# Kernel tuning notes

Measured on AMD Instinct MI355X. Metric: run time of the kernel, lower is better.

The kernel has to match this reference:

```python
import jax, jax.numpy as jnp
import numpy as np

B, C, D, J = 8, 2048, 128, 128

def setup_inputs() -> dict:
    key = jax.random.key(0)
    ks = jax.random.split(key, 24)
    s = 0.02
    inp = {
        "operation_features": jax.random.normal(ks[0], (B, C, D), jnp.float32),
        "relations": jax.random.randint(ks[1], (B, C - 2, 2), 0, C, jnp.int64),
        "begins_idx": jax.random.randint(ks[2], (B, J), 0, C, jnp.int64),
        "ends_idx": jax.random.randint(ks[3], (B, J), 0, C, jnp.int64),
        "same_type_mask": (jax.random.uniform(ks[4], (B, C, C)) > 0.5).astype(jnp.float32),
        # BeginEndEncoder
        "W_begin": jax.random.normal(ks[5], (D, D), jnp.float32) * s,
        "b_begin": jnp.zeros((D,), jnp.float32),
        "W_end": jax.random.normal(ks[6], (D, D), jnp.float32) * s,
        "b_end": jnp.zeros((D,), jnp.float32),
        # OperationTimeRelationEncoder.mix: Linear(3D -> D)
        "W_mix3": jax.random.normal(ks[7], (3 * D, D), jnp.float32) * s,
        "b_mix3": jnp.zeros((D,), jnp.float32),
        # SelfAttention (hidden_dim = D)
        "W_qkv": jax.random.normal(ks[8], (D, 3 * D), jnp.float32) * s,
        "b_qkv": jnp.zeros((3 * D,), jnp.float32),
        "w_score": jax.random.normal(ks[9], (2 * D,), jnp.float32) * s,
        "b_score": jnp.zeros((), jnp.float32),
        "W_out": jax.random.normal(ks[10], (D, D), jnp.float32) * s,
        "b_out": jnp.zeros((D,), jnp.float32),
        # block mix: Linear(2D -> D)
        "W_mix2": jax.random.normal(ks[11], (2 * D, D), jnp.float32) * s,
        "b_mix2": jnp.zeros((D,), jnp.float32),
    }
    return inp

def _gather_ops(ops, idx):
    # ops: [B,C,D], idx: [B,M] -> [B,M,D]  (torch.gather along dim 1 with expanded index)
    Bb, _, Dd = ops.shape
    M = idx.shape[1]
    return jnp.take_along_axis(ops, jnp.broadcast_to(idx[:, :, None], (Bb, M, Dd)), axis=1)

def reference(operation_features, relations, begins_idx, ends_idx, same_type_mask,
              W_begin, b_begin, W_end, b_end, W_mix3, b_mix3,
              W_qkv, b_qkv, w_score, b_score, W_out, b_out, W_mix2, b_mix2):
    ops = operation_features
    Dd = ops.shape[-1]
    # --- OperationTimeRelationEncoder ---
    pred = _gather_ops(ops, relations[..., 0])      # [B,C-2,D]
    succ = _gather_ops(ops, relations[..., 1])      # [B,C-2,D]
    concated = jnp.concatenate([ops[:, :-2, :], pred, succ], axis=-1)  # [B,C-2,3D]
    mixed = concated @ W_mix3 + b_mix3              # [B,C-2,D]
    begin_f = _gather_ops(ops, begins_idx) @ W_begin + b_begin  # [B,J,D]
    end_f = _gather_ops(ops, ends_idx) @ W_end + b_end
    begin = jnp.mean(begin_f, axis=1)               # [B,D]
    end = jnp.mean(end_f, axis=1)
    seq = jnp.concatenate([mixed, begin[:, None, :], end[:, None, :]], axis=1)  # [B,C,D]
    # --- SelfAttention (GAT-style additive score, decomposed to avoid CxCx2h blowup) ---
    qkv = ops @ W_qkv + b_qkv                       # [B,C,3D]
    q, k, v = jnp.split(qkv, 3, axis=-1)
    sq = q @ w_score[:Dd]                           # [B,C]  q_i . w_q
    sk = k @ w_score[Dd:]                           # [B,C]  k_j . w_k
    scores = jax.nn.leaky_relu(sq[:, :, None] + sk[:, None, :] + b_score)  # [B,C,C]
    attn = jax.nn.softmax(scores * same_type_mask, axis=-1)                # multiplicative mask, as in torch
    weighted = jnp.einsum('bij,bjd->bid', attn, v)  # [B,C,D]
    same_type = weighted @ W_out + b_out            # [B,C,D]
    # --- final mix ---
    return jnp.concatenate([seq, same_type], axis=-1) @ W_mix2 + b_mix2  # [B,C,D]
```

## Files before the change

### kernel.cpp

```cpp
#include <hip/hip_runtime.h>
#include <cstddef>

typedef __bf16 bf16;
typedef __bf16 bf16x4 __attribute__((ext_vector_type(4)));
typedef __bf16 bf16x8 __attribute__((ext_vector_type(8)));
typedef float  f32x4  __attribute__((ext_vector_type(4)));

#define MFMA16(a, b, c) __builtin_amdgcn_mfma_f32_16x16x32_bf16((a), (b), (c), 0, 0, 0)

#define BB 8
#define CC 2048
#define DD 128
#define JJN 128

#define WS_PK    ((size_t)0)
#define WS_OATT  ((size_t)4194304)
#define WS_OPS16 ((size_t)8388608)
#define WS_SQF   ((size_t)12582912)
#define WS_SKF   ((size_t)12648448)
#define WS_G1T   ((size_t)12713984)
#define WS_G2T   ((size_t)12746752)
#define WS_G3T   ((size_t)12779520)
#define WS_WCT   ((size_t)12812288)
#define WS_GBT   ((size_t)12845056)
#define WS_GET   ((size_t)12877824)
#define WS_UQK   ((size_t)12910592)
#define WS_BBM   ((size_t)12911104)
#define WS_BBB   ((size_t)12911616)
#define WS_BBE   ((size_t)12912128)
#define WS_SC    ((size_t)12912640)
#define WS_WCN   ((size_t)12913152)
#define WS_GBN   ((size_t)12945920)
#define WS_GEN   ((size_t)12978688)
#define WS_MB    ((size_t)13011456)
#define WS_MEANV ((size_t)17205760)

__global__ __launch_bounds__(256) void k_prepcast(
    const float* __restrict__ ops, bf16* __restrict__ ops16,
    const float* __restrict__ mask, const int* __restrict__ begins,
    const int* __restrict__ ends,
    const float* __restrict__ Wmix3, const float* __restrict__ Wmix2,
    const float* __restrict__ Wout,  const float* __restrict__ Wbegin,
    const float* __restrict__ Wend,  const float* __restrict__ Wqkv,
    const float* __restrict__ bqkv,  const float* __restrict__ wscore,
    const float* __restrict__ bscore,const float* __restrict__ bmix3,
    const float* __restrict__ bout,  const float* __restrict__ bmix2,
    const float* __restrict__ bbegin,const float* __restrict__ bend,
    bf16* __restrict__ G1T, bf16* __restrict__ G2T, bf16* __restrict__ G3T,
    bf16* __restrict__ WCT, bf16* __restrict__ GBT, bf16* __restrict__ GET,
    bf16* __restrict__ WCN, bf16* __restrict__ GBN, bf16* __restrict__ GEN,
    bf16* __restrict__ uqk, float* __restrict__ BBM, float* __restrict__ BBB,
    float* __restrict__ BBE, float* __restrict__ sc,
    unsigned char* __restrict__ MBITS, float* __restrict__ MEANV)
{
    __shared__ bf16  LshT[128 * 132];
    __shared__ float Rsh[128 * 8];
    int wg = blockIdx.x;
    int t  = threadIdx.x;

    if (wg == 0) {
        for (int half = 0; half < 2; ++half) {
            #pragma unroll
            for (int pass = 0; pass < 16; ++pass) {
                int idx = pass * 256 + t;
                int d   = idx >> 5;
                int e0  = (idx & 31) * 4;
                f32x4 v = *(const f32x4*)(Wqkv + d*384 + half*128 + e0);
                #pragma unroll
                for (int jj = 0; jj < 4; ++jj)
                    LshT[(e0 + jj)*132 + d] = (bf16)v[jj];
            }
            if (t < 32) {
                f32x4 wv = *(const f32x4*)(wscore + half*128 + t*4);
                #pragma unroll
                for (int jj = 0; jj < 4; ++jj) Rsh[t*4 + jj] = wv[jj];
            }
            __syncthreads();
            if (t < 128) {
                float s = 0.f;
                for (int e = 0; e < 128; ++e)
                    s += (float)LshT[e*132 + t] * Rsh[e];
                uqk[half*128 + t] = (bf16)s;
            }
            __syncthreads();
        }
        float bm = 0.f, bb_ = 0.f, be_ = 0.f, bon = 0.f;
        for (int half = 0; half < 2; ++half) {
            #pragma unroll
            for (int pass = 0; pass < 16; ++pass) {
                int idx = pass * 256 + t;
                int f   = idx >> 5;
                int e0  = (idx & 31) * 4;
                f32x4 v = *(const f32x4*)(Wmix2 + (size_t)(half*128 + f)*128 + e0);
                #pragma unroll
                for (int jj = 0; jj < 4; ++jj)
                    LshT[f*132 + e0 + jj] = (bf16)v[jj];
            }
            if (t < 32) {
                if (half == 0) {
                    f32x4 v0 = *(const f32x4*)(bmix3  + t*4);
                    f32x4 v1 = *(const f32x4*)(bbegin + t*4);
                    f32x4 v2 = *(const f32x4*)(bend   + t*4);
                    #pragma unroll
                    for (int jj = 0; jj < 4; ++jj) {
                        Rsh[t*4 + jj]       = v0[jj];
                        Rsh[128 + t*4 + jj] = v1[jj];
                        Rsh[256 + t*4 + jj] = v2[jj];
                    }
                } else {
                    f32x4 v3 = *(const f32x4*)(bout + t*4);
                    #pragma unroll
                    for (int jj = 0; jj < 4; ++jj) Rsh[t*4 + jj] = v3[jj];
                }
            }
            __syncthreads();
            if (t < 128) {
                if (half == 0) {
                    for (int f = 0; f < 128; ++f) {
                        float wv = (float)LshT[f*132 + t];
                        bm  += Rsh[f]       * wv;
                        bb_ += Rsh[128 + f] * wv;
                        be_ += Rsh[256 + f] * wv;
                    }
                } else {
                    for (int f = 0; f < 128; ++f)
                        bon += Rsh[f] * (float)LshT[f*132 + t];
                }
            }
            __syncthreads();
        }
        if (t < 128) {
            float bm2 = bmix2[t];
            BBM[t] = bm  + bon + bm2;
            BBB[t] = bb_ + bon + bm2;
            BBE[t] = be_ + bon + bm2;
        }
        if (t >= 128) {
            int e2 = t - 128;
            Rsh[512 + e2] = bqkv[e2]       * wscore[e2];
            Rsh[640 + e2] = bqkv[128 + e2] * wscore[128 + e2];
        }
        __syncthreads();
        if (t == 0) {
            float cq = 0.f, ck = 0.f;
            for (int e2 = 0; e2 < 128; ++e2) {
                cq += Rsh[512 + e2];
                ck += Rsh[640 + e2];
            }
            sc[0] = cq + bscore[0];
            sc[1] = ck;
        }
        return;
    }
    if (wg <= 16) {
        int task = wg - 1;
        int b2 = task >> 1, which = task & 1;
        const int* idxp = which ? (ends + b2 * JJN) : (begins + b2 * JJN);
        int* ish = (int*)Rsh;
        if (t < JJN) ish[t] = idxp[t];
        __syncthreads();
        int d = t & 127, half = t >> 7;
        const float* opsb = ops + (size_t)b2 * CC * DD;
        float s = 0.f;
        #pragma unroll 8
        for (int j = 0; j < 64; ++j) {
            int r = ish[half * 64 + j];
            s += opsb[(size_t)r * DD + d];
        }
        float* fsh = Rsh + 256;
        fsh[half * 128 + d] = s;
        __syncthreads();
        if (t < 128)
            MEANV[task * 128 + t] = (fsh[t] + fsh[128 + t]) * (1.0f / (float)JJN);
        return;
    }
    if (wg <= 2064) {
        int p = wg - 17;
        size_t base = (size_t)p * 16384;
        const float* mp = mask + base;
        unsigned char* ob = MBITS + (base >> 3);
        #pragma unroll
        for (int k = 0; k < 8; ++k) {
            size_t fo = (size_t)k * 2048 + (size_t)t * 8;
            f32x4 a = __builtin_nontemporal_load((const f32x4*)(mp + fo));
            f32x4 c = __builtin_nontemporal_load((const f32x4*)(mp + fo + 4));
            unsigned byte = 0;
            #pragma unroll
            for (int e = 0; e < 4; ++e) {
                byte |= (a[e] != 0.f ? 1u : 0u) << e;
                byte |= (c[e] != 0.f ? 1u : 0u) << (4 + e);
            }
            ob[k * 256 + t] = (unsigned char)byte;
        }
        return;
    }
    if (wg <= 2160) {
        int id  = wg - 2065;
        int mat = id >> 4, sub = id & 15;
        const float* L; const float* R; bf16* O; bf16* O2;
        switch (mat) {
            case 0: L = Wmix3;           R = Wmix2;           O = G1T; O2 = nullptr; break;
            case 1: L = Wmix3 + 128*128; R = Wmix2;           O = G2T; O2 = nullptr; break;
            case 2: L = Wmix3 + 256*128; R = Wmix2;           O = G3T; O2 = nullptr; break;
            case 3: L = Wout;            R = Wmix2 + 128*128; O = WCT; O2 = WCN; break;
            case 4: L = Wbegin;          R = Wmix2;           O = GBT; O2 = GBN; break;
            default:L = Wend;            R = Wmix2;           O = GET; O2 = GEN; break;
        }
        int e0 = sub * 8;
        #pragma unroll
        for (int pass = 0; pass < 16; ++pass) {
            int idx = pass * 256 + t;
            int d   = idx >> 5;
            int f0  = (idx & 31) * 4;
            f32x4 v = *(const f32x4*)(L + d * 128 + f0);
            #pragma unroll
            for (int jj = 0; jj < 4; ++jj)
                LshT[(f0 + jj) * 132 + d] = (bf16)v[jj];
        }
        #pragma unroll
        for (int pass = 0; pass < 4; ++pass) {
            int idx = pass * 256 + t;
            int f   = idx >> 3;
            int ee  = idx & 7;
            Rsh[f * 8 + ee] = R[f * 128 + e0 + ee];
        }
        __syncthreads();
        int ee = t >> 5;
        int e  = e0 + ee;
        int d0 = (t & 31) * 4;
        float s[4] = {0.f, 0.f, 0.f, 0.f};
        for (int f = 0; f < 128; ++f) {
            bf16x4 lv = *(const bf16x4*)&LshT[f * 132 + d0];
            float rv = Rsh[f * 8 + ee];
            #pragma unroll
            for (int dd = 0; dd < 4; ++dd)
                s[dd] += (float)lv[dd] * rv;
        }
        #pragma unroll
        for (int dd = 0; dd < 4; ++dd) {
            O[e * 128 + d0 + dd] = (bf16)s[dd];
            if (O2) O2[(d0 + dd) * 128 + e] = (bf16)s[dd];
        }
        return;
    }
    size_t i = (size_t)(wg - 2161) * 256 + t;
    f32x4 a = *(const f32x4*)(ops + i * 8);
    f32x4 b = *(const f32x4*)(ops + i * 8 + 4);
    bf16x8 o;
    #pragma unroll
    for (int e = 0; e < 4; ++e) { o[e] = (bf16)a[e]; o[4 + e] = (bf16)b[e]; }
    *(bf16x8*)(ops16 + i * 8) = o;
}

__global__ __launch_bounds__(256) void k_v(
    const bf16* __restrict__ ops16, const float* __restrict__ Wqkv,
    const float* __restrict__ bqkv, const bf16* __restrict__ uqk,
    const float* __restrict__ sc,
    bf16* __restrict__ PK, float* __restrict__ sqf, float* __restrict__ skf)
{
    __shared__ bf16 A[144 * 136];
    int b  = blockIdx.x >> 4;
    int jt = (blockIdx.x & 15) * 128;
    int t  = threadIdx.x;
    #pragma unroll
    for (int pass = 0; pass < 16; ++pass) {
        int idx = pass * 256 + t;
        int d   = idx >> 5;
        int n0  = (idx & 31) * 4;
        f32x4 v = *(const f32x4*)(Wqkv + d*384 + 256 + n0);
        #pragma unroll
        for (int jj = 0; jj < 4; ++jj)
            A[(n0 + jj)*136 + d] = (bf16)v[jj];
    }
    {
        int row = t >> 7, col = t & 127;
        A[(128 + row)*136 + col] = uqk[row*128 + col];
    }
    for (int idx = t; idx < 14*136; idx += 256)
        A[130*136 + idx] = (bf16)0.f;
    __syncthreads();

    int lane = t & 63, w = t >> 6;
    int m = lane & 15, q = lane >> 4;
    f32x4 acc[9][2];
    #pragma unroll
    for (int rb = 0; rb < 9; ++rb)
        #pragma unroll
        for (int cb = 0; cb < 2; ++cb)
            acc[rb][cb] = {0.f, 0.f, 0.f, 0.f};

    const bf16* opsb = ops16 + (size_t)b * CC * DD;
    #pragma unroll
    for (int kc = 0; kc < 4; ++kc) {
        bf16x8 bfr[2];
        #pragma unroll
        for (int cb = 0; cb < 2; ++cb) {
            int j = jt + w*32 + cb*16 + m;
            bfr[cb] = *(const bf16x8*)(opsb + (size_t)j*DD + kc*32 + q*8);
        }
        #pragma unroll
        for (int rb = 0; rb < 9; ++rb) {
            bf16x8 afr = *(const bf16x8*)&A[(rb*16 + m)*136 + kc*32 + q*8];
            acc[rb][0] = MFMA16(afr, bfr[0], acc[rb][0]);
            acc[rb][1] = MFMA16(afr, bfr[1], acc[rb][1]);
        }
    }
    float cqb = sc[0], ckv = sc[1];
    #pragma unroll
    for (int cb = 0; cb < 2; ++cb) {
        int j = jt + w*32 + cb*16 + m;
        if (q == 0) {
            sqf[b*CC + j] = acc[8][cb][0] + cqb;
            skf[b*CC + j] = acc[8][cb][1] + ckv;
        }
    }
    __syncthreads();
    bf16* pack = A;
    #pragma unroll
    for (int cb = 0; cb < 2; ++cb) {
        int qq_base = cb*2 + (m>>3);
        int e       = m & 7;
        #pragma unroll
        for (int rb = 0; rb < 8; ++rb) {
            #pragma unroll
            for (int r = 0; r < 4; ++r) {
                float v = acc[rb][cb][r] + bqkv[256 + rb*16 + q*4 + r];
                pack[w*4096 + rb*512 + qq_base*128 + (q*4+r)*8 + e] = (bf16)v;
            }
        }
    }
    __syncthreads();
    bf16* pkb = PK + (size_t)b * DD * CC + (size_t)jt * 128;
    #pragma unroll
    for (int pass = 0; pass < 8; ++pass) {
        int lidx = pass * 256 + t;
        *(uint4*)(pkb + (size_t)lidx * 8) = *(const uint4*)&pack[lidx * 8];
    }
}

__device__ __forceinline__ void load_vb(const bf16* __restrict__ pkb, int jc,
                                        int q, int m, bf16x8 vb[8])
{
    #pragma unroll
    for (int nb = 0; nb < 8; ++nb)
        vb[nb] = *(const bf16x8*)(pkb + ((size_t)(((jc*8 + nb)*4 + q)*16 + m)) * 8);
}

__device__ __forceinline__ void substep(const float* __restrict__ skb,
    unsigned mbyte, int st, int sub, int q, float sq,
    const bf16x8 vb[8], float& lsum, f32x4 acc[8])
{
    int jo = st * 64 + sub * 32 + q * 8;
    f32x4 s0 = *(const f32x4*)(skb + jo);
    f32x4 s1 = *(const f32x4*)(skb + jo + 4);
    float sks[8] = {s0[0], s0[1], s0[2], s0[3], s1[0], s1[1], s1[2], s1[3]};
    bf16x8 a;
    #pragma unroll
    for (int e = 0; e < 8; ++e) {
        float tv = sq + sks[e];
        float lr = fmaxf(tv, 0.01f * tv);
        float pm = (float)((mbyte >> e) & 1u);
        float p  = __expf(lr * pm);
        lsum += p;
        a[e] = (bf16)p;
    }
    #pragma unroll
    for (int nb = 0; nb < 8; ++nb)
        acc[nb] = MFMA16(a, vb[nb], acc[nb]);
}

__global__ __launch_bounds__(256) void k_attepi(
    const unsigned char* __restrict__ MBITS, const bf16* __restrict__ PK,
    const float* __restrict__ sqf, const float* __restrict__ skf,
    const bf16* __restrict__ ops16, const int* __restrict__ relations,
    const bf16* __restrict__ G1T, const bf16* __restrict__ G2T,
    const bf16* __restrict__ G3T, const bf16* __restrict__ WCT,
    const bf16* __restrict__ GBN, const bf16* __restrict__ GEN,
    const bf16* __restrict__ WCN,
    const float* __restrict__ BBM, const float* __restrict__ BBB,
    const float* __restrict__ BBE, const float* __restrict__ MEANV,
    float* __restrict__ out)
{
    __shared__ __align__(16) char smem[52224];
    int t    = threadIdx.x;
    int lane = t & 63, w = t >> 6;
    int b    = blockIdx.x & 7;
    int i0   = (blockIdx.x >> 3) << 5;
    int m = lane & 15, q = lane >> 4;

    unsigned char* Lb  = (unsigned char*)smem;
    float*         skb = (float*)(smem + 8704 + w * 2048);

    {
        int row = t >> 3, seg = t & 7;
        const uint4* src = (const uint4*)(MBITS
            + ((size_t)(b * CC + i0 + row)) * 256 + seg * 32);
        uint4 v0 = src[0], v1 = src[1];
        *(uint4*)(Lb + row * 272 + seg * 32)      = v0;
        *(uint4*)(Lb + row * 272 + seg * 32 + 16) = v1;
    }
    {
        const float* src = skf + b * CC + w * 512;
        f32x4 v0 = *(const f32x4*)(src + lane * 4);
        f32x4 v1 = *(const f32x4*)(src + 256 + lane * 4);
        *(f32x4*)(skb + lane * 4)       = v0;
        *(f32x4*)(skb + 256 + lane * 4) = v1;
    }
    float sq0 = sqf[b * CC + i0 + m];
    float sq1 = sqf[b * CC + i0 + 16 + m];
    const bf16* pkb = PK + (size_t)b * DD * CC;
    int jc0 = w * 16;

    f32x4 acc0[8], acc1[8];
    #pragma unroll
    for (int nb = 0; nb < 8; ++nb) {
        acc0[nb] = {0.f, 0.f, 0.f, 0.f};
        acc1[nb] = {0.f, 0.f, 0.f, 0.f};
    }
    float lsum0 = 0.f, lsum1 = 0.f;
    __syncthreads();

    for (int st = 0; st < 8; ++st) {
        #pragma unroll
        for (int sub = 0; sub < 2; ++sub) {
            bf16x8 vb[8];
            load_vb(pkb, jc0 + st * 2 + sub, q, m, vb);
            int bo = w * 64 + st * 8 + sub * 4 + q;
            unsigned mb0 = Lb[m * 272 + bo];
            unsigned mb1 = Lb[(16 + m) * 272 + bo];
            substep(skb, mb0, st, sub, q, sq0, vb, lsum0, acc0);
            substep(skb, mb1, st, sub, q, sq1, vb, lsum1, acc1);
        }
    }

    __syncthreads();
    float* Osh  = (float*)(smem + 8704);
    float* Lsh  = (float*)(smem + 42496);
    bf16*  Obuf = (bf16*)(smem + 43520);
    #pragma unroll
    for (int tile = 0; tile < 2; ++tile) {
        float ls = tile ? lsum1 : lsum0;
        ls += __shfl_xor(ls, 16, 64);
        ls += __shfl_xor(ls, 32, 64);
        if (q == 0) Lsh[w * 16 + m] = ls;
        const f32x4* acc = tile ? acc1 : acc0;
        #pragma unroll
        for (int nb = 0; nb < 8; ++nb)
            #pragma unroll
            for (int r = 0; r < 4; ++r)
                Osh[(w * 16 + q * 4 + r) * 132 + nb * 16 + m] = acc[nb][r];
        __syncthreads();

        int r   = t >> 4;
        int c0e = (t & 15) * 8;
        float l = Lsh[r] + Lsh[16 + r] + Lsh[32 + r] + Lsh[48 + r];
        float inv = 1.0f / l;
        bf16x8 o;
        #pragma unroll
        for (int e = 0; e < 8; ++e) {
            float s = Osh[r * 132 + c0e + e] + Osh[(16 + r) * 132 + c0e + e]
                    + Osh[(32 + r) * 132 + c0e + e] + Osh[(48 + r) * 132 + c0e + e];
            o[e] = (bf16)(s * inv);
        }
        *(bf16x8*)&Obuf[(tile * 16 + r) * 136 + c0e] = o;
        __syncthreads();
    }

    bf16* Abuf = (bf16*)smem;
    bf16* Bbuf = (bf16*)(smem + 8704);

    f32x4 eacc[2][2];
    #pragma unroll
    for (int rb = 0; rb < 2; ++rb)
        #pragma unroll
        for (int cb = 0; cb < 2; ++cb)
            eacc[rb][cb] = {0.f, 0.f, 0.f, 0.f};

    const bf16* Bsrc[4] = {G1T, G2T, G3T, WCT};
    int arow = t >> 3, ao = (t & 7) * 16;
    int brow = t >> 1, bo2 = (t & 1) * 64;
    int c = i0 + arow;

    for (int term = 0; term < 4; ++term) {
        if (term < 3) {
            const bf16* src;
            if (term == 0) src = ops16 + ((size_t)(b * CC + c)) * DD;
            else {
                int ridx = relations[((size_t)b * (CC - 2) + min(c, CC - 3)) * 2 + (term - 1)];
                src = ops16 + ((size_t)(b * CC) + ridx) * DD;
            }
            *(uint4*)&Abuf[arow * 136 + ao]     = *(const uint4*)(src + ao);
            *(uint4*)&Abuf[arow * 136 + ao + 8] = *(const uint4*)(src + ao + 8);
        }
        const uint4* bs = (const uint4*)(Bsrc[term] + brow * 128 + bo2);
        uint4* bd = (uint4*)&Bbuf[brow * 136 + bo2];
        #pragma unroll
        for (int ii = 0; ii < 8; ++ii) bd[ii] = bs[ii];
        __syncthreads();

        const bf16* Asrc = (term == 3) ? Obuf : Abuf;
        #pragma unroll
        for (int kc = 0; kc < 4; ++kc) {
            bf16x8 bfr[2];
            #pragma unroll
            for (int cb = 0; cb < 2; ++cb)
                bfr[cb] = *(const bf16x8*)&Bbuf[(w * 32 + cb * 16 + m) * 136 + kc * 32 + q * 8];
            #pragma unroll
            for (int rb = 0; rb < 2; ++rb) {
                bf16x8 afr = *(const bf16x8*)&Asrc[(rb * 16 + m) * 136 + kc * 32 + q * 8];
                eacc[rb][0] = MFMA16(afr, bfr[0], eacc[rb][0]);
                eacc[rb][1] = MFMA16(afr, bfr[1], eacc[rb][1]);
            }
        }
        __syncthreads();
    }
    #pragma unroll
    for (int cb = 0; cb < 2; ++cb) {
        int col = w * 32 + cb * 16 + m;
        float bias = BBM[col];
        #pragma unroll
        for (int rb = 0; rb < 2; ++rb) {
            #pragma unroll
            for (int r = 0; r < 4; ++r) {
                int cg = i0 + rb * 16 + q * 4 + r;
                if (cg < CC - 2)
                    out[((size_t)(b * CC) + cg) * DD + col] = eacc[rb][cb][r] + bias;
            }
        }
    }

    if (i0 == CC - 32) {
        __syncthreads();
        float* mv2 = (float*)smem;
        int grp = t >> 7, tl = t & 127;
        mv2[grp * 128 + tl] = MEANV[((size_t)b * 2 + grp) * 128 + tl];
        __syncthreads();
        int which = grp;
        const bf16* G    = which ? GEN : GBN;
        const float* Bv  = which ? BBE : BBB;
        const bf16* orow = Obuf + (30 + which) * 136;
        float a = Bv[tl];
        const float* mv = mv2 + grp * 128;
        for (int d = 0; d < 128; ++d) {
            a += mv[d] * (float)G[d * 128 + tl];
            a += (float)orow[d] * (float)WCN[d * 128 + tl];
        }
        out[((size_t)b * CC + (CC - 2 + which)) * DD + tl] = a;
    }
}

extern "C" void kernel_launch(void* const* d_in, const int* in_sizes, int n_in,
                              void* d_out, int out_size, void* d_ws, size_t ws_size,
                              hipStream_t stream)
{
    const float* ops      = (const float*)d_in[0];
    const int*  relations = (const int*)d_in[1];
    const int*  begins    = (const int*)d_in[2];
    const int*  ends      = (const int*)d_in[3];
    const float* mask     = (const float*)d_in[4];
    const float* Wbegin   = (const float*)d_in[5];
    const float* bbegin   = (const float*)d_in[6];
    const float* Wend     = (const float*)d_in[7];
    const float* bend     = (const float*)d_in[8];
    const float* Wmix3    = (const float*)d_in[9];
    const float* bmix3    = (const float*)d_in[10];
    const float* Wqkv     = (const float*)d_in[11];
    const float* bqkv     = (const float*)d_in[12];
    const float* wscore   = (const float*)d_in[13];
    const float* bscore   = (const float*)d_in[14];
    const float* Wout     = (const float*)d_in[15];
    const float* bout     = (const float*)d_in[16];
    const float* Wmix2    = (const float*)d_in[17];
    const float* bmix2    = (const float*)d_in[18];
    float* outp = (float*)d_out;

    char* ws = (char*)d_ws;
    bf16*  PK    = (bf16*)(ws + WS_PK);
    bf16*  OPS16 = (bf16*)(ws + WS_OPS16);
    float* sqf   = (float*)(ws + WS_SQF);
    float* skf   = (float*)(ws + WS_SKF);
    bf16*  G1T   = (bf16*)(ws + WS_G1T);
    bf16*  G2T   = (bf16*)(ws + WS_G2T);
    bf16*  G3T   = (bf16*)(ws + WS_G3T);
    bf16*  WCT   = (bf16*)(ws + WS_WCT);
    bf16*  GBT   = (bf16*)(ws + WS_GBT);
    bf16*  GET   = (bf16*)(ws + WS_GET);
    bf16*  WCN   = (bf16*)(ws + WS_WCN);
    bf16*  GBN   = (bf16*)(ws + WS_GBN);
    bf16*  GEN   = (bf16*)(ws + WS_GEN);
    bf16*  UQK   = (bf16*)(ws + WS_UQK);
    float* BBM   = (float*)(ws + WS_BBM);
    float* BBB   = (float*)(ws + WS_BBB);
    float* BBE   = (float*)(ws + WS_BBE);
    float* SC    = (float*)(ws + WS_SC);
    unsigned char* MBITS = (unsigned char*)(ws + WS_MB);
    float* MEANV = (float*)(ws + WS_MEANV);

    k_prepcast<<<dim3(3185), dim3(256), 0, stream>>>(
        ops, OPS16, mask, begins, ends,
        Wmix3, Wmix2, Wout, Wbegin, Wend, Wqkv, bqkv, wscore, bscore,
        bmix3, bout, bmix2, bbegin, bend,
        G1T, G2T, G3T, WCT, GBT, GET, WCN, GBN, GEN,
        UQK, BBM, BBB, BBE, SC, MBITS, MEANV);

    k_v<<<dim3(128), dim3(256), 0, stream>>>(
        OPS16, Wqkv, bqkv, UQK, SC, PK, sqf, skf);

    k_attepi<<<dim3(512), dim3(256), 0, stream>>>(
        MBITS, PK, sqf, skf, OPS16, relations,
        G1T, G2T, G3T, WCT, GBN, GEN, WCN, BBM, BBB, BBE, MEANV, outp);
}
```

Baseline: 275.2 us.

## Stream fp32 mask directly into attention kernel with register-staged double buffering

Removes the separate mask-to-bitmask pass in the prep kernel and instead has the attention kernel read the fp32 same_type_mask directly. Each wave prefetches mask tiles two stages ahead into registers, converts them to bf16 and writes them into a per-wave double-buffered LDS region consumed by the score computation. This avoids writing and re-reading the packed bitmask and shrinks the prep grid. In exchange the attention kernel carries more register pressure and more LDS, and it now depends on overlapping the large mask read with compute. The mask is also now applied as a multiplicative bf16 value instead of a 0/1 bit.

```diff
diff --git a/kernel.cpp b/kernel.cpp
--- a/kernel.cpp
+++ b/kernel.cpp
@@ -14,7 +14,6 @@
 #define JJN 128
 
 #define WS_PK    ((size_t)0)
-#define WS_OATT  ((size_t)4194304)
 #define WS_OPS16 ((size_t)8388608)
 #define WS_SQF   ((size_t)12582912)
 #define WS_SKF   ((size_t)12648448)
@@ -32,13 +31,11 @@
 #define WS_WCN   ((size_t)12913152)
 #define WS_GBN   ((size_t)12945920)
 #define WS_GEN   ((size_t)12978688)
-#define WS_MB    ((size_t)13011456)
 #define WS_MEANV ((size_t)17205760)
 
 __global__ __launch_bounds__(256) void k_prepcast(
     const float* __restrict__ ops, bf16* __restrict__ ops16,
-    const float* __restrict__ mask, const int* __restrict__ begins,
-    const int* __restrict__ ends,
+    const int* __restrict__ begins, const int* __restrict__ ends,
     const float* __restrict__ Wmix3, const float* __restrict__ Wmix2,
     const float* __restrict__ Wout,  const float* __restrict__ Wbegin,
     const float* __restrict__ Wend,  const float* __restrict__ Wqkv,
@@ -50,8 +47,7 @@
     bf16* __restrict__ WCT, bf16* __restrict__ GBT, bf16* __restrict__ GET,
     bf16* __restrict__ WCN, bf16* __restrict__ GBN, bf16* __restrict__ GEN,
     bf16* __restrict__ uqk, float* __restrict__ BBM, float* __restrict__ BBB,
-    float* __restrict__ BBE, float* __restrict__ sc,
-    unsigned char* __restrict__ MBITS, float* __restrict__ MEANV)
+    float* __restrict__ BBE, float* __restrict__ sc, float* __restrict__ MEANV)
 {
     __shared__ bf16  LshT[128 * 132];
     __shared__ float Rsh[128 * 8];
@@ -174,28 +170,8 @@
             MEANV[task * 128 + t] = (fsh[t] + fsh[128 + t]) * (1.0f / (float)JJN);
         return;
     }
-    if (wg <= 2064) {
-        int p = wg - 17;
-        size_t base = (size_t)p * 16384;
-        const float* mp = mask + base;
-        unsigned char* ob = MBITS + (base >> 3);
-        #pragma unroll
-        for (int k = 0; k < 8; ++k) {
-            size_t fo = (size_t)k * 2048 + (size_t)t * 8;
-            f32x4 a = __builtin_nontemporal_load((const f32x4*)(mp + fo));
-            f32x4 c = __builtin_nontemporal_load((const f32x4*)(mp + fo + 4));
-            unsigned byte = 0;
-            #pragma unroll
-            for (int e = 0; e < 4; ++e) {
-                byte |= (a[e] != 0.f ? 1u : 0u) << e;
-                byte |= (c[e] != 0.f ? 1u : 0u) << (4 + e);
-            }
-            ob[k * 256 + t] = (unsigned char)byte;
-        }
-        return;
-    }
-    if (wg <= 2160) {
-        int id  = wg - 2065;
+    if (wg <= 112) {
+        int id  = wg - 17;
         int mat = id >> 4, sub = id & 15;
         const float* L; const float* R; bf16* O; bf16* O2;
         switch (mat) {
@@ -243,7 +219,7 @@
         }
         return;
     }
-    size_t i = (size_t)(wg - 2161) * 256 + t;
+    size_t i = (size_t)(wg - 113) * 256 + t;
     f32x4 a = *(const f32x4*)(ops + i * 8);
     f32x4 b = *(const f32x4*)(ops + i * 8 + 4);
     bf16x8 o;
@@ -338,6 +314,35 @@
     }
 }
 
+struct MaskLd { f32x4 v[8]; };
+
+__device__ __forceinline__ MaskLd stage_load(const float* __restrict__ mrow0,
+                                             int st, int lane)
+{
+    MaskLd L;
+    int rr0 = lane >> 4, cc = (lane & 15) * 4;
+    const float* src = mrow0 + st * 64 + cc;
+    #pragma unroll
+    for (int k = 0; k < 8; ++k)
+        L.v[k] = __builtin_nontemporal_load(
+            (const f32x4*)(src + ((size_t)(rr0 + k * 4)) * CC));
+    return L;
+}
+
+__device__ __forceinline__ void stage_write(const MaskLd& L, bf16* mb,
+                                            int buf, int lane)
+{
+    int rr0 = lane >> 4, cc = (lane & 15) * 4;
+    bf16* dst = mb + buf * 2816;
+    #pragma unroll
+    for (int k = 0; k < 8; ++k) {
+        bf16x4 o;
+        #pragma unroll
+        for (int e = 0; e < 4; ++e) o[e] = (bf16)L.v[k][e];
+        *(bf16x4*)(dst + (rr0 + k * 4) * 88 + cc) = o;
+    }
+}
+
 __device__ __forceinline__ void load_vb(const bf16* __restrict__ pkb, int jc,
                                         int q, int m, bf16x8 vb[8])
 {
@@ -346,10 +351,12 @@
         vb[nb] = *(const bf16x8*)(pkb + ((size_t)(((jc*8 + nb)*4 + q)*16 + m)) * 8);
 }
 
-__device__ __forceinline__ void substep(const float* __restrict__ skb,
-    unsigned mbyte, int st, int sub, int q, float sq,
+__device__ __forceinline__ void substep(const bf16* mb, const float* skb,
+    int buf, int st, int sub, int tile, int q, int m, float sq,
     const bf16x8 vb[8], float& lsum, f32x4 acc[8])
 {
+    bf16x8 mk = *(const bf16x8*)(mb + buf * 2816 + (tile*16 + m) * 88
+                                 + sub * 32 + q * 8);
     int jo = st * 64 + sub * 32 + q * 8;
     f32x4 s0 = *(const f32x4*)(skb + jo);
     f32x4 s1 = *(const f32x4*)(skb + jo + 4);
@@ -359,8 +366,8 @@
     for (int e = 0; e < 8; ++e) {
         float tv = sq + sks[e];
         float lr = fmaxf(tv, 0.01f * tv);
-        float pm = (float)((mbyte >> e) & 1u);
-        float p  = __expf(lr * pm);
+        float z  = lr * (float)mk[e];
+        float p  = __expf(z);
         lsum += p;
         a[e] = (bf16)p;
     }
@@ -370,7 +377,7 @@
 }
 
 __global__ __launch_bounds__(256) void k_attepi(
-    const unsigned char* __restrict__ MBITS, const bf16* __restrict__ PK,
+    const float* __restrict__ mask, const bf16* __restrict__ PK,
     const float* __restrict__ sqf, const float* __restrict__ skf,
     const bf16* __restrict__ ops16, const int* __restrict__ relations,
     const bf16* __restrict__ G1T, const bf16* __restrict__ G2T,
@@ -381,34 +388,27 @@
     const float* __restrict__ BBE, const float* __restrict__ MEANV,
     float* __restrict__ out)
 {
-    __shared__ __align__(16) char smem[52224];
+    __shared__ __align__(16) char smem[53248];
     int t    = threadIdx.x;
     int lane = t & 63, w = t >> 6;
     int b    = blockIdx.x & 7;
     int i0   = (blockIdx.x >> 3) << 5;
     int m = lane & 15, q = lane >> 4;
 
-    unsigned char* Lb  = (unsigned char*)smem;
-    float*         skb = (float*)(smem + 8704 + w * 2048);
+    bf16*  mbuf = (bf16*)(smem + w * 11264);
+    float* skb  = (float*)(smem + 45056 + w * 2048);
 
     {
-        int row = t >> 3, seg = t & 7;
-        const uint4* src = (const uint4*)(MBITS
-            + ((size_t)(b * CC + i0 + row)) * 256 + seg * 32);
-        uint4 v0 = src[0], v1 = src[1];
-        *(uint4*)(Lb + row * 272 + seg * 32)      = v0;
-        *(uint4*)(Lb + row * 272 + seg * 32 + 16) = v1;
-    }
-    {
-        const float* src = skf + b * CC + w * 512;
-        f32x4 v0 = *(const f32x4*)(src + lane * 4);
-        f32x4 v1 = *(const f32x4*)(src + 256 + lane * 4);
-        *(f32x4*)(skb + lane * 4)       = v0;
-        *(f32x4*)(skb + 256 + lane * 4) = v1;
-    }
-    float sq0 = sqf[b * CC + i0 + m];
-    float sq1 = sqf[b * CC + i0 + 16 + m];
-    const bf16* pkb = PK + (size_t)b * DD * CC;
+        const float* src = skf + b*CC + w*512;
+        f32x4 v0 = *(const f32x4*)(src + lane*4);
+        f32x4 v1 = *(const f32x4*)(src + 256 + lane*4);
+        *(f32x4*)(skb + lane*4) = v0;
+        *(f32x4*)(skb + 256 + lane*4) = v1;
+    }
+    float sq0 = sqf[b*CC + i0 + m];
+    float sq1 = sqf[b*CC + i0 + 16 + m];
+    const float* mrow0 = mask + ((size_t)(b*CC + i0))*CC + w*512;
+    const bf16*  pkb   = PK + (size_t)b * DD * CC;
     int jc0 = w * 16;
 
     f32x4 acc0[8], acc1[8];
@@ -418,24 +418,30 @@
         acc1[nb] = {0.f, 0.f, 0.f, 0.f};
     }
     float lsum0 = 0.f, lsum1 = 0.f;
-    __syncthreads();
-
+
+    {   MaskLd r0 = stage_load(mrow0, 0, lane);
+        stage_write(r0, mbuf, 0, lane); }
+    MaskLd r1 = stage_load(mrow0, 1, lane);
+    MaskLd r2 = stage_load(mrow0, 2, lane);
+
+    int buf = 0;
     for (int st = 0; st < 8; ++st) {
         #pragma unroll
         for (int sub = 0; sub < 2; ++sub) {
             bf16x8 vb[8];
-            load_vb(pkb, jc0 + st * 2 + sub, q, m, vb);
-            int bo = w * 64 + st * 8 + sub * 4 + q;
-            unsigned mb0 = Lb[m * 272 + bo];
-            unsigned mb1 = Lb[(16 + m) * 272 + bo];
-            substep(skb, mb0, st, sub, q, sq0, vb, lsum0, acc0);
-            substep(skb, mb1, st, sub, q, sq1, vb, lsum1, acc1);
-        }
+            load_vb(pkb, jc0 + st*2 + sub, q, m, vb);
+            substep(mbuf, skb, buf, st, sub, 0, q, m, sq0, vb, lsum0, acc0);
+            substep(mbuf, skb, buf, st, sub, 1, q, m, sq1, vb, lsum1, acc1);
+        }
+        if (st + 1 < 8) stage_write(r1, mbuf, buf ^ 1, lane);
+        r1 = r2;
+        if (st + 3 < 8) r2 = stage_load(mrow0, st + 3, lane);
+        buf ^= 1;
     }
 
     __syncthreads();
-    float* Osh  = (float*)(smem + 8704);
-    float* Lsh  = (float*)(smem + 42496);
+    float* Osh  = (float*)smem;
+    float* Lsh  = (float*)(smem + 33792);
     bf16*  Obuf = (bf16*)(smem + 43520);
     #pragma unroll
     for (int tile = 0; tile < 2; ++tile) {
@@ -593,20 +599,19 @@
     float* BBB   = (float*)(ws + WS_BBB);
     float* BBE   = (float*)(ws + WS_BBE);
     float* SC    = (float*)(ws + WS_SC);
-    unsigned char* MBITS = (unsigned char*)(ws + WS_MB);
     float* MEANV = (float*)(ws + WS_MEANV);
 
-    k_prepcast<<<dim3(3185), dim3(256), 0, stream>>>(
-        ops, OPS16, mask, begins, ends,
+    k_prepcast<<<dim3(1137), dim3(256), 0, stream>>>(
+        ops, OPS16, begins, ends,
         Wmix3, Wmix2, Wout, Wbegin, Wend, Wqkv, bqkv, wscore, bscore,
         bmix3, bout, bmix2, bbegin, bend,
         G1T, G2T, G3T, WCT, GBT, GET, WCN, GBN, GEN,
-        UQK, BBM, BBB, BBE, SC, MBITS, MEANV);
+        UQK, BBM, BBB, BBE, SC, MEANV);
 
     k_v<<<dim3(128), dim3(256), 0, stream>>>(
         OPS16, Wqkv, bqkv, UQK, SC, PK, sqf, skf);
 
     k_attepi<<<dim3(512), dim3(256), 0, stream>>>(
-        MBITS, PK, sqf, skf, OPS16, relations,
+        mask, PK, sqf, skf, OPS16, relations,
         G1T, G2T, G3T, WCT, GBN, GEN, WCN, BBM, BBB, BBE, MEANV, outp);
 }
```

Result: slower. 283.8 us (+3.1%).

## Halve k_v tile to double grid and double-buffer V loads in attention loop

Applied to the files above, without the earlier changes.

k_v now processes 64 columns per block instead of 128, launching 256 blocks rather than 128 so more of the GPU's compute units are occupied. Each block still rebuilds the same weight tile in shared memory, so that staging work is repeated twice as often. The attention kernel's inner loop is fully unrolled and double-buffers the packed V fragments, loading the next chunk while the current one is used in MFMAs to hide global load latency. The price is higher register pressure from two sets of V fragments.

```diff
diff --git a/kernel.cpp b/kernel.cpp
--- a/kernel.cpp
+++ b/kernel.cpp
@@ -14,7 +14,6 @@
 #define JJN 128
 
 #define WS_PK    ((size_t)0)
-#define WS_OATT  ((size_t)4194304)
 #define WS_OPS16 ((size_t)8388608)
 #define WS_SQF   ((size_t)12582912)
 #define WS_SKF   ((size_t)12648448)
@@ -259,8 +258,8 @@
     bf16* __restrict__ PK, float* __restrict__ sqf, float* __restrict__ skf)
 {
     __shared__ bf16 A[144 * 136];
-    int b  = blockIdx.x >> 4;
-    int jt = (blockIdx.x & 15) * 128;
+    int b  = blockIdx.x & 7;
+    int jt = (blockIdx.x >> 3) * 64;
     int t  = threadIdx.x;
     #pragma unroll
     for (int pass = 0; pass < 16; ++pass) {
@@ -282,57 +281,45 @@
 
     int lane = t & 63, w = t >> 6;
     int m = lane & 15, q = lane >> 4;
-    f32x4 acc[9][2];
-    #pragma unroll
-    for (int rb = 0; rb < 9; ++rb)
-        #pragma unroll
-        for (int cb = 0; cb < 2; ++cb)
-            acc[rb][cb] = {0.f, 0.f, 0.f, 0.f};
+    f32x4 acc[9];
+    #pragma unroll
+    for (int rb = 0; rb < 9; ++rb) acc[rb] = {0.f, 0.f, 0.f, 0.f};
 
     const bf16* opsb = ops16 + (size_t)b * CC * DD;
+    int j = jt + w*16 + m;
     #pragma unroll
     for (int kc = 0; kc < 4; ++kc) {
-        bf16x8 bfr[2];
-        #pragma unroll
-        for (int cb = 0; cb < 2; ++cb) {
-            int j = jt + w*32 + cb*16 + m;
-            bfr[cb] = *(const bf16x8*)(opsb + (size_t)j*DD + kc*32 + q*8);
-        }
+        bf16x8 bfr = *(const bf16x8*)(opsb + (size_t)j*DD + kc*32 + q*8);
         #pragma unroll
         for (int rb = 0; rb < 9; ++rb) {
             bf16x8 afr = *(const bf16x8*)&A[(rb*16 + m)*136 + kc*32 + q*8];
-            acc[rb][0] = MFMA16(afr, bfr[0], acc[rb][0]);
-            acc[rb][1] = MFMA16(afr, bfr[1], acc[rb][1]);
+            acc[rb] = MFMA16(afr, bfr, acc[rb]);
         }
     }
     float cqb = sc[0], ckv = sc[1];
-    #pragma unroll
-    for (int cb = 0; cb < 2; ++cb) {
-        int j = jt + w*32 + cb*16 + m;
-        if (q == 0) {
-            sqf[b*CC + j] = acc[8][cb][0] + cqb;
-            skf[b*CC + j] = acc[8][cb][1] + ckv;
-        }
+    if (q == 0) {
+        sqf[b*CC + j] = acc[8][0] + cqb;
+        skf[b*CC + j] = acc[8][1] + ckv;
     }
     __syncthreads();
     bf16* pack = A;
-    #pragma unroll
-    for (int cb = 0; cb < 2; ++cb) {
-        int qq_base = cb*2 + (m>>3);
-        int e       = m & 7;
+    {
+        int jcl = w >> 1;
+        int qv  = (w & 1) * 2 + (m >> 3);
+        int ev  = m & 7;
         #pragma unroll
         for (int rb = 0; rb < 8; ++rb) {
             #pragma unroll
             for (int r = 0; r < 4; ++r) {
-                float v = acc[rb][cb][r] + bqkv[256 + rb*16 + q*4 + r];
-                pack[w*4096 + rb*512 + qq_base*128 + (q*4+r)*8 + e] = (bf16)v;
+                float v = acc[rb][r] + bqkv[256 + rb*16 + q*4 + r];
+                pack[jcl*4096 + rb*512 + qv*128 + (q*4+r)*8 + ev] = (bf16)v;
             }
         }
     }
     __syncthreads();
     bf16* pkb = PK + (size_t)b * DD * CC + (size_t)jt * 128;
     #pragma unroll
-    for (int pass = 0; pass < 8; ++pass) {
+    for (int pass = 0; pass < 4; ++pass) {
         int lidx = pass * 256 + t;
         *(uint4*)(pkb + (size_t)lidx * 8) = *(const uint4*)&pack[lidx * 8];
     }
@@ -346,13 +333,12 @@
         vb[nb] = *(const bf16x8*)(pkb + ((size_t)(((jc*8 + nb)*4 + q)*16 + m)) * 8);
 }
 
-__device__ __forceinline__ void substep(const float* __restrict__ skb,
-    unsigned mbyte, int st, int sub, int q, float sq,
+__device__ __forceinline__ void substep(const float* __restrict__ skw,
+    unsigned mbyte, int jo, float sq,
     const bf16x8 vb[8], float& lsum, f32x4 acc[8])
 {
-    int jo = st * 64 + sub * 32 + q * 8;
-    f32x4 s0 = *(const f32x4*)(skb + jo);
-    f32x4 s1 = *(const f32x4*)(skb + jo + 4);
+    f32x4 s0 = *(const f32x4*)(skw + jo);
+    f32x4 s1 = *(const f32x4*)(skw + jo + 4);
     float sks[8] = {s0[0], s0[1], s0[2], s0[3], s1[0], s1[1], s1[2], s1[3]};
     bf16x8 a;
     #pragma unroll
@@ -389,7 +375,7 @@
     int m = lane & 15, q = lane >> 4;
 
     unsigned char* Lb  = (unsigned char*)smem;
-    float*         skb = (float*)(smem + 8704 + w * 2048);
+    float*         skw = (float*)(smem + 8704 + w * 2048);
 
     {
         int row = t >> 3, seg = t & 7;
@@ -401,10 +387,8 @@
     }
     {
         const float* src = skf + b * CC + w * 512;
-        f32x4 v0 = *(const f32x4*)(src + lane * 4);
-        f32x4 v1 = *(const f32x4*)(src + 256 + lane * 4);
-        *(f32x4*)(skb + lane * 4)       = v0;
-        *(f32x4*)(skb + 256 + lane * 4) = v1;
+        *(f32x4*)(skw + lane * 4)       = *(const f32x4*)(src + lane * 4);
+        *(f32x4*)(skw + 256 + lane * 4) = *(const f32x4*)(src + 256 + lane * 4);
     }
     float sq0 = sqf[b * CC + i0 + m];
     float sq1 = sqf[b * CC + i0 + 16 + m];
@@ -420,16 +404,25 @@
     float lsum0 = 0.f, lsum1 = 0.f;
     __syncthreads();
 
-    for (int st = 0; st < 8; ++st) {
-        #pragma unroll
-        for (int sub = 0; sub < 2; ++sub) {
-            bf16x8 vb[8];
-            load_vb(pkb, jc0 + st * 2 + sub, q, m, vb);
-            int bo = w * 64 + st * 8 + sub * 4 + q;
+    bf16x8 vbA[8], vbB[8];
+    load_vb(pkb, jc0, q, m, vbA);
+    #pragma unroll
+    for (int c = 0; c < 16; c += 2) {
+        load_vb(pkb, jc0 + c + 1, q, m, vbB);
+        {
+            int bo = w * 64 + c * 4 + q;
             unsigned mb0 = Lb[m * 272 + bo];
             unsigned mb1 = Lb[(16 + m) * 272 + bo];
-            substep(skb, mb0, st, sub, q, sq0, vb, lsum0, acc0);
-            substep(skb, mb1, st, sub, q, sq1, vb, lsum1, acc1);
+            substep(skw, mb0, c * 32 + q * 8, sq0, vbA, lsum0, acc0);
+            substep(skw, mb1, c * 32 + q * 8, sq1, vbA, lsum1, acc1);
+        }
+        if (c + 2 < 16) load_vb(pkb, jc0 + c + 2, q, m, vbA);
+        {
+            int bo = w * 64 + (c + 1) * 4 + q;
+            unsigned mb0 = Lb[m * 272 + bo];
+            unsigned mb1 = Lb[(16 + m) * 272 + bo];
+            substep(skw, mb0, (c + 1) * 32 + q * 8, sq0, vbB, lsum0, acc0);
+            substep(skw, mb1, (c + 1) * 32 + q * 8, sq1, vbB, lsum1, acc1);
         }
     }
 
@@ -603,7 +596,7 @@
         G1T, G2T, G3T, WCT, GBT, GET, WCN, GBN, GEN,
         UQK, BBM, BBB, BBE, SC, MBITS, MEANV);
 
-    k_v<<<dim3(128), dim3(256), 0, stream>>>(
+    k_v<<<dim3(256), dim3(256), 0, stream>>>(
         OPS16, Wqkv, bqkv, UQK, SC, PK, sqf, skf);
 
     k_attepi<<<dim3(512), dim3(256), 0, stream>>>(
```

Measured after the change: 279.8 us. No clear change (+1.7%).
